# Kernel tuning notes

Measured on AMD Instinct MI355X. Metric: run time of the kernel, lower is better.

The kernel has to match this reference:

```python
import jax, jax.numpy as jnp
from jax import lax
import numpy as np

N_STEPS = 21

def _conv3x3(a, w):
    # NCHW input, OIHW weight, stride 1, padding 1 ('same' for 3x3)
    return lax.conv_general_dilated(
        a, w, window_strides=(1, 1), padding=[(1, 1), (1, 1)],
        dimension_numbers=('NCHW', 'OIHW', 'NCHW'))

def setup_inputs() -> dict:
    key = jax.random.key(0)
    x = jax.random.normal(key, (32, 1, 1024, 1024), dtype=jnp.float32)
    convAx = jnp.array([[[[0.2538, 0.5022, 0.07344],
                          [0.17864, 1.0622, 0.24616],
                          [0.2454, 0.90548, 0.52616]]]], dtype=jnp.float32)
    convBx = jnp.array([[[[-0.083, -3.15852, 3.24172],
                          [-2.0894, -9.34624, -2.0018],
                          [6.889, -1.53384, 7.71856]]]], dtype=jnp.float32)
    biasx = jnp.array([-0.07002], dtype=jnp.float32)
    return {"x": x, "convAx": convAx, "convBx": convBx, "biasx": biasx}

def reference(x, convAx, convBx, biasx):
    # global min-max normalization to [-1, 1]
    xmin = jnp.min(x)
    xmax = jnp.max(x)
    xn = (x - xmin) * (2.0 / (xmax - xmin)) - 1.0
    # fixed drive term
    BU = _conv3x3(xn, convBx)  # [B,1,H,W]
    bias = biasx.reshape(1, -1, 1, 1)
    s0 = jnp.zeros_like(xn)

    def step(s, _):
        s = _conv3x3(s, convAx) + bias + BU
        s = jnp.clip(s, -1.0, 1.0)  # activeFun = hard clamp to [-1,1]
        return s, None

    s, _ = lax.scan(step, s0, None, length=N_STEPS)
    return (s + 1.0) * 0.5
```

## Files before the change

kernel.cpp:

```cpp
#include <hip/hip_runtime.h>

#define HW 1024
#define NIMG 32
#define IMGPX ((size_t)HW * HW)
#define NELEM (NIMG * IMGPX)

typedef float f2 __attribute__((ext_vector_type(2)));

#define RING 6
#define TOX 116
#define TOY 52
#define NBX 9
#define NBY 20
#define LSTR 136
#define SLOTS 34
#define BUFW (SLOTS * LSTR)

__device__ __forceinline__ unsigned f2su(float f) {
    unsigned u = __float_as_uint(f);
    return (u & 0x80000000u) ? ~u : (u | 0x80000000u);
}
__device__ __forceinline__ float s2f(unsigned u) {
    return __uint_as_float((u & 0x80000000u) ? (u & 0x7fffffffu) : ~u);
}

__global__ void mm_init(unsigned* mm) {
    mm[0] = 0xFFFFFFFFu;
    mm[1] = 0u;
}

__global__ __launch_bounds__(256) void mm_reduce(const float4* __restrict__ x,
                                                 unsigned* mm, int n4) {
    const int tid = threadIdx.x;
    int gid = blockIdx.x * blockDim.x + tid;
    const int stride = gridDim.x * blockDim.x;
    float vmin = 3.4e38f, vmax = -3.4e38f;
    for (int i = gid; i < n4; i += stride) {
        float4 v = x[i];
        vmin = fminf(vmin, fminf(fminf(v.x, v.y), fminf(v.z, v.w)));
        vmax = fmaxf(vmax, fmaxf(fmaxf(v.x, v.y), fmaxf(v.z, v.w)));
    }
    __shared__ float smin[256];
    __shared__ float smax[256];
    smin[tid] = vmin; smax[tid] = vmax;
    __syncthreads();
    for (int s = 128; s > 0; s >>= 1) {
        if (tid < s) {
            smin[tid] = fminf(smin[tid], smin[tid + s]);
            smax[tid] = fmaxf(smax[tid], smax[tid + s]);
        }
        __syncthreads();
    }
    if (tid == 0) {
        atomicMin(&mm[0], f2su(smin[0]));
        atomicMax(&mm[1], f2su(smax[0]));
    }
}

struct RowW { f2 P[2]; float L, R; };

template <int FIRST, int LAST>
__global__ __launch_bounds__(512) void fused_k(
    const float* __restrict__ x, const float* __restrict__ sin_,
    float* __restrict__ sout, const unsigned* __restrict__ mm,
    const float* __restrict__ wAp, const float* __restrict__ wBp,
    const float* __restrict__ biasp) {
#pragma clang fp contract(off)
    __shared__ float sb[2 * BUFW];
    const int tid = threadIdx.x;
    const int tx = tid & 31;
    const int tyg = tid >> 5;
    const int lane = tid & 63;
    const int laneL = (lane + 63) & 63;
    const int laneR = (lane + 1) & 63;
    const int r0 = tyg << 2;
    const int c0 = tx << 2;
    const int bx = (int)blockIdx.x, by = (int)blockIdx.y;
    const int ox = bx * TOX - RING;
    const int oy = by * TOY - RING;
    const size_t img = (size_t)blockIdx.z * IMGPX;
    const bool edgeX = (bx == 0) | (bx == NBX - 1);
    const bool edgeY = (by == 0) | (by == NBY - 1);
    const bool intr = !(edgeX | edgeY);

    const float xmin = s2f(mm[0]);
    const float xmax = s2f(mm[1]);
    const float scale = 2.0f / (xmax - xmin);
    const float b = biasp[0];

    auto ldSlot = [&](int wb) -> RowW {
        RowW o;
        const float4 q0 = *reinterpret_cast<const float4*>(&sb[wb + c0]);
        o.P[0] = f2{q0.x, q0.y}; o.P[1] = f2{q0.z, q0.w};
        const float fromL = __shfl(q0.w, laneL);
        const float fromR = __shfl(q0.x, laneR);
        o.L = (tx == 0) ? sb[wb + 130] : fromL;
        o.R = (tx == 31) ? sb[wb + 131] : fromR;
        return o;
    };

    float cf[9];
    auto conv9 = [&](const RowW& A, const RowW& B, const RowW& C, int p) -> f2 {
#pragma clang fp contract(off)
        f2 acc = f2{0.0f, 0.0f};
        f2 tl, tr;
        tl = f2{(p == 0) ? A.L : A.P[0].y, A.P[p].x};
        tr = f2{A.P[p].y, (p == 0) ? A.P[1].x : A.R};
        acc = acc + f2{cf[0], cf[0]} * tl;
        acc = acc + f2{cf[1], cf[1]} * A.P[p];
        acc = acc + f2{cf[2], cf[2]} * tr;
        tl = f2{(p == 0) ? B.L : B.P[0].y, B.P[p].x};
        tr = f2{B.P[p].y, (p == 0) ? B.P[1].x : B.R};
        acc = acc + f2{cf[3], cf[3]} * tl;
        acc = acc + f2{cf[4], cf[4]} * B.P[p];
        acc = acc + f2{cf[5], cf[5]} * tr;
        tl = f2{(p == 0) ? C.L : C.P[0].y, C.P[p].x};
        tr = f2{C.P[p].y, (p == 0) ? C.P[1].x : C.R};
        acc = acc + f2{cf[6], cf[6]} * tl;
        acc = acc + f2{cf[7], cf[7]} * C.P[p];
        acc = acc + f2{cf[8], cf[8]} * tr;
        return acc;
    };

    if (intr) {
        for (int k = tid; k < 66 * 130; k += 512) {
            const int si = k / 130;
            const int cc = (k - si * 130) - 1;
            const int w = (cc == -1) ? 130 : ((cc == 128) ? 131 : cc);
            const float v =
                (x[img + (size_t)(oy + si - 1) * HW + (ox + cc)] - xmin) * scale - 1.0f;
            sb[si * LSTR + w] = v;
        }
    } else {
        for (int k = tid; k < 66 * 130; k += 512) {
            const int si = k / 130;
            const int cc = (k - si * 130) - 1;
            const int w = (cc == -1) ? 130 : ((cc == 128) ? 131 : cc);
            const int gr = oy + si - 1;
            const int gc = ox + cc;
            float v = 0.0f;
            if (gr >= 0 && gr < HW && gc >= 0 && gc < HW)
                v = (x[img + (size_t)gr * HW + gc] - xmin) * scale - 1.0f;
            sb[si * LSTR + w] = v;
        }
    }
    __syncthreads();

#pragma unroll
    for (int i = 0; i < 9; ++i) cf[i] = wBp[i];
    f2 bu[4][2];
    {
        RowW prev = ldSlot((r0) * LSTR);
        RowW cur = ldSlot((r0 + 1) * LSTR);
#pragma unroll
        for (int i = 0; i < 4; ++i) {
            RowW nxt = ldSlot((r0 + 2 + i) * LSTR);
            bu[i][0] = conv9(prev, cur, nxt, 0);
            bu[i][1] = conv9(prev, cur, nxt, 1);
            prev = cur; cur = nxt;
        }
    }
    __syncthreads();

    f2 res[4][2];
    float hS[4];
    for (int k = tid; k < 324; k += 512) {
        int rr, cc;
        if (k < 260) { rr = (k < 130) ? -1 : 64; cc = (k % 130) - 1; }
        else {
            const int kk = k - 260;
            const int s = kk >> 1;
            rr = (s & 1) ? ((s >> 1) * 4 + 3) : ((s >> 1) * 4);
            cc = (kk & 1) ? 128 : -1;
        }
        const int w = (cc == -1) ? 130 : ((cc == 128) ? 131 : cc);
        const int slot = (rr == -1) ? 0 : ((rr == 64) ? 33 : ((rr >> 2) * 2 + 1 + (((rr & 3) == 3) ? 1 : 0)));
        float v = 0.0f;
        if (!FIRST) {
            const int gr = oy + rr, gc = ox + cc;
            if (gr >= 0 && gr < HW && gc >= 0 && gc < HW)
                v = sin_[img + (size_t)gr * HW + gc];
        }
        const int wo = slot * LSTR + w;
        sb[wo] = v;
        sb[BUFW + wo] = v;
    }
    if (FIRST) {
#pragma unroll
        for (int i = 0; i < 4; ++i) {
            hS[i] = 0.0f;
            res[i][0] = f2{0.0f, 0.0f};
            res[i][1] = f2{0.0f, 0.0f};
        }
    } else if (intr) {
#pragma unroll
        for (int i = 0; i < 4; ++i) {
            const float2* src = reinterpret_cast<const float2*>(
                &sin_[img + (size_t)(oy + r0 + i) * HW + ox + c0]);
            const float2 t0 = src[0];
            const float2 t1 = src[1];
            res[i][0] = f2{t0.x, t0.y};
            res[i][1] = f2{t1.x, t1.y};
            float hv = 0.0f;
            if (tx == 0) hv = sin_[img + (size_t)(oy + r0 + i) * HW + (ox - 1)];
            else if (tx == 31) hv = sin_[img + (size_t)(oy + r0 + i) * HW + (ox + 128)];
            hS[i] = hv;
        }
    } else {
#pragma unroll
        for (int i = 0; i < 4; ++i) {
            const int gr = oy + r0 + i;
            const bool rin = (gr >= 0) & (gr < HW);
#pragma unroll
            for (int cl = 0; cl < 4; ++cl) {
                const int gc = ox + c0 + cl;
                float v = 0.0f;
                if (rin && gc >= 0 && gc < HW) v = sin_[img + (size_t)gr * HW + gc];
                res[i][cl >> 1][cl & 1] = v;
            }
            float hv = 0.0f;
            if (tx == 0) {
                const int gc = ox - 1;
                if (rin && gc >= 0) hv = sin_[img + (size_t)gr * HW + gc];
            } else if (tx == 31) {
                const int gc = ox + 128;
                if (rin && gc < HW) hv = sin_[img + (size_t)gr * HW + gc];
            }
            hS[i] = hv;
        }
    }

    auto wrRow = [&](int bo, int i, int slot) {
        *reinterpret_cast<float4*>(&sb[bo + slot * LSTR + c0]) =
            make_float4(res[i][0].x, res[i][0].y, res[i][1].x, res[i][1].y);
    };
    wrRow(0, 0, 2 * tyg + 1);
    wrRow(0, 3, 2 * tyg + 2);
    __syncthreads();

#pragma unroll
    for (int i = 0; i < 9; ++i) cf[i] = wAp[i];
    float mR[4];
#pragma unroll
    for (int i = 0; i < 4; ++i) {
        const int g = oy + r0 + i;
        mR[i] = (g >= 0 && g < HW) ? 1.0f : 0.0f;
    }
    f2 mC2[2];
#pragma unroll
    for (int p = 0; p < 2; ++p) {
        const int g0 = ox + c0 + 2 * p, g1 = g0 + 1;
        mC2[p] = f2{(g0 >= 0 && g0 < HW) ? 1.0f : 0.0f,
                    (g1 >= 0 && g1 < HW) ? 1.0f : 0.0f};
    }

    auto buildRow = [&](const f2 pr[2], float hs) -> RowW {
        RowW o;
        o.P[0] = pr[0]; o.P[1] = pr[1];
        const float fromL = __shfl(pr[1].y, laneL);
        const float fromR = __shfl(pr[0].x, laneR);
        o.L = (tx == 0) ? hs : fromL;
        o.R = (tx == 31) ? hs : fromR;
        return o;
    };

    auto stepRow = [&](int i, const RowW& A, const RowW& B, const RowW& C) {
        f2 n0 = conv9(A, B, C, 0);
        f2 n1 = conv9(A, B, C, 1);
        n0 = (n0 + f2{b, b}) + bu[i][0];
        n1 = (n1 + f2{b, b}) + bu[i][1];
        n0 = __builtin_elementwise_max(n0, f2{-1.0f, -1.0f});
        n0 = __builtin_elementwise_min(n0, f2{1.0f, 1.0f});
        n1 = __builtin_elementwise_max(n1, f2{-1.0f, -1.0f});
        n1 = __builtin_elementwise_min(n1, f2{1.0f, 1.0f});
        if (!intr) {
            n0 = n0 * f2{mR[i], mR[i]};
            n1 = n1 * f2{mR[i], mR[i]};
            n0 = n0 * mC2[0];
            n1 = n1 * mC2[1];
        }
        res[i][0] = n0; res[i][1] = n1;
    };

    const int slotM1 = (tyg == 0) ? 0 : 2 * tyg;
    const int slotP4 = (tyg == 15) ? 33 : 2 * tyg + 3;

#pragma unroll 1
    for (int t = 0; t < 7; ++t) {
        const int rdo = (t & 1) * BUFW;
        const int wro = BUFW - rdo;
        const RowW m1 = ldSlot(rdo + slotM1 * LSTR);
        const RowW p4 = ldSlot(rdo + slotP4 * LSTR);
        const RowW o0 = buildRow(res[0], hS[0]);
        const RowW o1 = buildRow(res[1], hS[1]);
        const RowW o2 = buildRow(res[2], hS[2]);
        const RowW o3 = buildRow(res[3], hS[3]);
        stepRow(0, m1, o0, o1);
        stepRow(3, o2, o3, p4);
        wrRow(wro, 0, 2 * tyg + 1);
        wrRow(wro, 3, 2 * tyg + 2);
        __syncthreads();
        stepRow(1, o0, o1, o2);
        stepRow(2, o1, o2, o3);
    }

    const bool fullc = intr && (c0 >= RING) && (c0 + 3 < RING + TOX);
#pragma unroll
    for (int i = 0; i < 4; ++i) {
        const int r = r0 + i;
        if (r < RING || r >= RING + TOY) continue;
        const int gr = oy + r;
        if (gr >= HW) continue;
        if (fullc) {
            float2* dst = reinterpret_cast<float2*>(&sout[img + (size_t)gr * HW + ox + c0]);
            f2 v0 = res[i][0], v1 = res[i][1];
            if (LAST) {
                v0 = (v0 + f2{1.0f, 1.0f}) * f2{0.5f, 0.5f};
                v1 = (v1 + f2{1.0f, 1.0f}) * f2{0.5f, 0.5f};
            }
            dst[0] = make_float2(v0.x, v0.y);
            dst[1] = make_float2(v1.x, v1.y);
        } else {
#pragma unroll
            for (int cl = 0; cl < 4; ++cl) {
                const int c = c0 + cl;
                if (c < RING || c >= RING + TOX) continue;
                const int gc = ox + c;
                if (gc < 0 || gc >= HW) continue;
                float v = res[i][cl >> 1][cl & 1];
                if (LAST) v = (v + 1.0f) * 0.5f;
                sout[img + (size_t)gr * HW + gc] = v;
            }
        }
    }
}

extern "C" void kernel_launch(void* const* d_in, const int* in_sizes, int n_in,
                              void* d_out, int out_size, void* d_ws, size_t ws_size,
                              hipStream_t stream) {
    const float* x = (const float*)d_in[0];
    const float* wA = (const float*)d_in[1];
    const float* wB = (const float*)d_in[2];
    const float* bias = (const float*)d_in[3];
    float* out = (float*)d_out;
    unsigned* mm = (unsigned*)d_ws;
    float* pong = (float*)((char*)d_ws + 1024);

    mm_init<<<1, 1, 0, stream>>>(mm);
    mm_reduce<<<2048, 256, 0, stream>>>((const float4*)x, mm, (int)(NELEM / 4));

    dim3 grid(NBX, NBY, NIMG);
    fused_k<1, 0><<<grid, 512, 0, stream>>>(x, nullptr, out, mm, wA, wB, bias);
    fused_k<0, 0><<<grid, 512, 0, stream>>>(x, out, pong, mm, wA, wB, bias);
    fused_k<0, 1><<<grid, 512, 0, stream>>>(x, pong, out, mm, wA, wB, bias);
}
```

Measured before the change: 822.4 us.

## Cache BU drive term in workspace and skip first zero-state step

```diff
diff --git a/kernel.cpp b/kernel.cpp
--- a/kernel.cpp
+++ b/kernel.cpp
@@ -59,10 +59,11 @@
 
 struct RowW { f2 P[2]; float L, R; };
 
-template <int FIRST, int LAST>
+template <int FIRST, int LAST, int BUMODE>
 __global__ __launch_bounds__(512) void fused_k(
     const float* __restrict__ x, const float* __restrict__ sin_,
-    float* __restrict__ sout, const unsigned* __restrict__ mm,
+    float* __restrict__ sout, float* __restrict__ bup,
+    const unsigned* __restrict__ mm,
     const float* __restrict__ wAp, const float* __restrict__ wBp,
     const float* __restrict__ biasp) {
 #pragma clang fp contract(off)
@@ -82,11 +83,27 @@
     const bool edgeX = (bx == 0) | (bx == NBX - 1);
     const bool edgeY = (by == 0) | (by == NBY - 1);
     const bool intr = !(edgeX | edgeY);
+    const bool fullc = intr && (c0 >= RING) && (c0 + 3 < RING + TOX);
 
     const float xmin = s2f(mm[0]);
     const float xmax = s2f(mm[1]);
     const float scale = 2.0f / (xmax - xmin);
     const float b = biasp[0];
+    const f2 b2 = f2{b, b};
+
+    float mR[4];
+#pragma unroll
+    for (int i = 0; i < 4; ++i) {
+        const int g = oy + r0 + i;
+        mR[i] = (g >= 0 && g < HW) ? 1.0f : 0.0f;
+    }
+    f2 mC2[2];
+#pragma unroll
+    for (int p = 0; p < 2; ++p) {
+        const int g0 = ox + c0 + 2 * p, g1 = g0 + 1;
+        mC2[p] = f2{(g0 >= 0 && g0 < HW) ? 1.0f : 0.0f,
+                    (g1 >= 0 && g1 < HW) ? 1.0f : 0.0f};
+    }
 
     auto ldSlot = [&](int wb) -> RowW {
         RowW o;
@@ -122,45 +139,93 @@
         return acc;
     };
 
-    if (intr) {
-        for (int k = tid; k < 66 * 130; k += 512) {
-            const int si = k / 130;
-            const int cc = (k - si * 130) - 1;
-            const int w = (cc == -1) ? 130 : ((cc == 128) ? 131 : cc);
-            const float v =
-                (x[img + (size_t)(oy + si - 1) * HW + (ox + cc)] - xmin) * scale - 1.0f;
-            sb[si * LSTR + w] = v;
+    f2 bu[4][2];
+
+    if (BUMODE != 2) {
+        if (intr) {
+            for (int k = tid; k < 66 * 130; k += 512) {
+                const int si = k / 130;
+                const int cc = (k - si * 130) - 1;
+                const int w = (cc == -1) ? 130 : ((cc == 128) ? 131 : cc);
+                const float v =
+                    (x[img + (size_t)(oy + si - 1) * HW + (ox + cc)] - xmin) * scale - 1.0f;
+                sb[si * LSTR + w] = v;
+            }
+        } else {
+            for (int k = tid; k < 66 * 130; k += 512) {
+                const int si = k / 130;
+                const int cc = (k - si * 130) - 1;
+                const int w = (cc == -1) ? 130 : ((cc == 128) ? 131 : cc);
+                const int gr = oy + si - 1;
+                const int gc = ox + cc;
+                float v = 0.0f;
+                if (gr >= 0 && gr < HW && gc >= 0 && gc < HW)
+                    v = (x[img + (size_t)gr * HW + gc] - xmin) * scale - 1.0f;
+                sb[si * LSTR + w] = v;
+            }
+        }
+        __syncthreads();
+
+#pragma unroll
+        for (int i = 0; i < 9; ++i) cf[i] = wBp[i];
+        {
+            RowW prev = ldSlot((r0) * LSTR);
+            RowW cur = ldSlot((r0 + 1) * LSTR);
+#pragma unroll
+            for (int i = 0; i < 4; ++i) {
+                RowW nxt = ldSlot((r0 + 2 + i) * LSTR);
+                bu[i][0] = conv9(prev, cur, nxt, 0);
+                bu[i][1] = conv9(prev, cur, nxt, 1);
+                prev = cur; cur = nxt;
+            }
+        }
+        __syncthreads();
+
+        if (BUMODE == 1) {
+#pragma unroll
+            for (int i = 0; i < 4; ++i) {
+                const int r = r0 + i;
+                if (r < RING || r >= RING + TOY) continue;
+                const int gr = oy + r;
+                if (gr >= HW) continue;
+                if (fullc) {
+                    *reinterpret_cast<float4*>(&bup[img + (size_t)gr * HW + ox + c0]) =
+                        make_float4(bu[i][0].x, bu[i][0].y, bu[i][1].x, bu[i][1].y);
+                } else {
+#pragma unroll
+                    for (int cl = 0; cl < 4; ++cl) {
+                        const int c = c0 + cl;
+                        if (c < RING || c >= RING + TOX) continue;
+                        const int gc = ox + c;
+                        if (gc < 0 || gc >= HW) continue;
+                        bup[img + (size_t)gr * HW + gc] = bu[i][cl >> 1][cl & 1];
+                    }
+                }
+            }
         }
     } else {
-        for (int k = tid; k < 66 * 130; k += 512) {
-            const int si = k / 130;
-            const int cc = (k - si * 130) - 1;
-            const int w = (cc == -1) ? 130 : ((cc == 128) ? 131 : cc);
-            const int gr = oy + si - 1;
-            const int gc = ox + cc;
-            float v = 0.0f;
-            if (gr >= 0 && gr < HW && gc >= 0 && gc < HW)
-                v = (x[img + (size_t)gr * HW + gc] - xmin) * scale - 1.0f;
-            sb[si * LSTR + w] = v;
-        }
-    }
-    __syncthreads();
-
-#pragma unroll
-    for (int i = 0; i < 9; ++i) cf[i] = wBp[i];
-    f2 bu[4][2];
-    {
-        RowW prev = ldSlot((r0) * LSTR);
-        RowW cur = ldSlot((r0 + 1) * LSTR);
-#pragma unroll
-        for (int i = 0; i < 4; ++i) {
-            RowW nxt = ldSlot((r0 + 2 + i) * LSTR);
-            bu[i][0] = conv9(prev, cur, nxt, 0);
-            bu[i][1] = conv9(prev, cur, nxt, 1);
-            prev = cur; cur = nxt;
-        }
-    }
-    __syncthreads();
+        if (intr) {
+#pragma unroll
+            for (int i = 0; i < 4; ++i) {
+                const float4 q = *reinterpret_cast<const float4*>(
+                    &bup[img + (size_t)(oy + r0 + i) * HW + ox + c0]);
+                bu[i][0] = f2{q.x, q.y};
+                bu[i][1] = f2{q.z, q.w};
+            }
+        } else {
+#pragma unroll
+            for (int i = 0; i < 4; ++i) {
+                int gr = oy + r0 + i;
+                gr = (gr < 0) ? 0 : ((gr >= HW) ? HW - 1 : gr);
+#pragma unroll
+                for (int cl = 0; cl < 4; ++cl) {
+                    int gc = ox + c0 + cl;
+                    gc = (gc < 0) ? 0 : ((gc >= HW) ? HW - 1 : gc);
+                    bu[i][cl >> 1][cl & 1] = bup[img + (size_t)gr * HW + gc];
+                }
+            }
+        }
+    }
 
     f2 res[4][2];
     float hS[4];
@@ -189,8 +254,17 @@
 #pragma unroll
         for (int i = 0; i < 4; ++i) {
             hS[i] = 0.0f;
-            res[i][0] = f2{0.0f, 0.0f};
-            res[i][1] = f2{0.0f, 0.0f};
+#pragma unroll
+            for (int p = 0; p < 2; ++p) {
+                f2 v = b2 + bu[i][p];
+                v = __builtin_elementwise_max(v, f2{-1.0f, -1.0f});
+                v = __builtin_elementwise_min(v, f2{1.0f, 1.0f});
+                if (!intr) {
+                    v = v * f2{mR[i], mR[i]};
+                    v = v * mC2[p];
+                }
+                res[i][p] = v;
+            }
         }
     } else if (intr) {
 #pragma unroll
@@ -240,19 +314,6 @@
 
 #pragma unroll
     for (int i = 0; i < 9; ++i) cf[i] = wAp[i];
-    float mR[4];
-#pragma unroll
-    for (int i = 0; i < 4; ++i) {
-        const int g = oy + r0 + i;
-        mR[i] = (g >= 0 && g < HW) ? 1.0f : 0.0f;
-    }
-    f2 mC2[2];
-#pragma unroll
-    for (int p = 0; p < 2; ++p) {
-        const int g0 = ox + c0 + 2 * p, g1 = g0 + 1;
-        mC2[p] = f2{(g0 >= 0 && g0 < HW) ? 1.0f : 0.0f,
-                    (g1 >= 0 && g1 < HW) ? 1.0f : 0.0f};
-    }
 
     auto buildRow = [&](const f2 pr[2], float hs) -> RowW {
         RowW o;
@@ -267,8 +328,8 @@
     auto stepRow = [&](int i, const RowW& A, const RowW& B, const RowW& C) {
         f2 n0 = conv9(A, B, C, 0);
         f2 n1 = conv9(A, B, C, 1);
-        n0 = (n0 + f2{b, b}) + bu[i][0];
-        n1 = (n1 + f2{b, b}) + bu[i][1];
+        n0 = (n0 + b2) + bu[i][0];
+        n1 = (n1 + b2) + bu[i][1];
         n0 = __builtin_elementwise_max(n0, f2{-1.0f, -1.0f});
         n0 = __builtin_elementwise_min(n0, f2{1.0f, 1.0f});
         n1 = __builtin_elementwise_max(n1, f2{-1.0f, -1.0f});
@@ -284,9 +345,10 @@
 
     const int slotM1 = (tyg == 0) ? 0 : 2 * tyg;
     const int slotP4 = (tyg == 15) ? 33 : 2 * tyg + 3;
+    const int NST = FIRST ? 6 : 7;
 
 #pragma unroll 1
-    for (int t = 0; t < 7; ++t) {
+    for (int t = 0; t < NST; ++t) {
         const int rdo = (t & 1) * BUFW;
         const int wro = BUFW - rdo;
         const RowW m1 = ldSlot(rdo + slotM1 * LSTR);
@@ -304,7 +366,6 @@
         stepRow(2, o1, o2, o3);
     }
 
-    const bool fullc = intr && (c0 >= RING) && (c0 + 3 < RING + TOX);
 #pragma unroll
     for (int i = 0; i < 4; ++i) {
         const int r = r0 + i;
@@ -345,12 +406,20 @@
     float* out = (float*)d_out;
     unsigned* mm = (unsigned*)d_ws;
     float* pong = (float*)((char*)d_ws + 1024);
+    float* bub = pong + NELEM;
 
     mm_init<<<1, 1, 0, stream>>>(mm);
     mm_reduce<<<2048, 256, 0, stream>>>((const float4*)x, mm, (int)(NELEM / 4));
 
     dim3 grid(NBX, NBY, NIMG);
-    fused_k<1, 0><<<grid, 512, 0, stream>>>(x, nullptr, out, mm, wA, wB, bias);
-    fused_k<0, 0><<<grid, 512, 0, stream>>>(x, out, pong, mm, wA, wB, bias);
-    fused_k<0, 1><<<grid, 512, 0, stream>>>(x, pong, out, mm, wA, wB, bias);
-}
+    const size_t needBU = 1024 + 2ull * NELEM * sizeof(float);
+    if (ws_size >= needBU) {
+        fused_k<1, 0, 1><<<grid, 512, 0, stream>>>(x, nullptr, out, bub, mm, wA, wB, bias);
+        fused_k<0, 0, 2><<<grid, 512, 0, stream>>>(x, out, pong, bub, mm, wA, wB, bias);
+        fused_k<0, 1, 2><<<grid, 512, 0, stream>>>(x, pong, out, bub, mm, wA, wB, bias);
+    } else {
+        fused_k<1, 0, 0><<<grid, 512, 0, stream>>>(x, nullptr, out, nullptr, mm, wA, wB, bias);
+        fused_k<0, 0, 0><<<grid, 512, 0, stream>>>(x, out, pong, nullptr, mm, wA, wB, bias);
+        fused_k<0, 1, 0><<<grid, 512, 0, stream>>>(x, pong, out, nullptr, mm, wA, wB, bias);
+    }
+}
```

Result: faster. 695.3 us, median of 2 (-15.5%).
